# Optimization experiments

Measured on AMD Instinct MI355X. Metric: run time of the kernel, lower is better.

The kernel has to match this reference:

```python
import jax, jax.numpy as jnp
import numpy as np

B, N, D, H, DH = 1, 192, 128, 4, 32
INNER = H * DH  # == D


def _ln(x, g, b):
    mu = x.mean(-1, keepdims=True)
    var = ((x - mu) ** 2).mean(-1, keepdims=True)
    return (x - mu) * jax.lax.rsqrt(var + 1e-5) * g + b


def _axial(x, row, lng, lnb, wq, wkv, wo, bo, wg, bg, wb):
    # x: (B, N, N, D). row=True: attend along axis 2 (rows as batch);
    # row=False: attend along axis 1 (columns as batch).
    scale = DH ** -0.5
    # edge bias from RAW x (edges are not layer-normed in the torch code)
    bias = jnp.einsum('bijd,dh->bhij', x, wb)            # (B, H, N, N)
    xn = _ln(x, lng, lnb)
    xa = xn if row else jnp.swapaxes(xn, 1, 2)           # (B, R, S, D)
    q = (xa @ wq).reshape(B, N, N, H, DH) * scale
    kv = (xa @ wkv).reshape(B, N, N, 2, H, DH)           # chunk(2): k then v
    k, v = kv[..., 0, :, :], kv[..., 1, :, :]
    # scores: (B, R, H, q, k); same bias matrix broadcast over every row/col R
    dots = jnp.einsum('brqhe,brkhe->brhqk', q, k) + bias[:, None]
    attn = jax.nn.softmax(dots, axis=-1)
    o = jnp.einsum('brhqk,brkhe->brqhe', attn, v).reshape(B, N, N, INNER)
    gates = jax.nn.sigmoid(xa @ wg + bg)                 # sigmoid gating on pre-attn x
    out = (o * gates) @ wo + bo
    return out if row else jnp.swapaxes(out, 1, 2)


def setup_inputs() -> dict:
    key = jax.random.key(0)
    ks = iter(jax.random.split(key, 32))

    def w(shape, s=0.02):
        return jax.random.normal(next(ks), shape, dtype=jnp.float32) * s

    inp = {"x": jax.random.normal(next(ks), (B, N, N, D), dtype=jnp.float32)}
    for sfx in ("o", "i"):  # outgoing (row) / ingoing (col) triangle attention
        inp[f"lng_{sfx}"] = jnp.ones((D,), jnp.float32)
        inp[f"lnb_{sfx}"] = jnp.zeros((D,), jnp.float32)
        inp[f"wq_{sfx}"] = w((D, INNER))
        inp[f"wkv_{sfx}"] = w((D, 2 * INNER))
        inp[f"wo_{sfx}"] = w((INNER, D))
        inp[f"bo_{sfx}"] = jnp.zeros((D,), jnp.float32)
        inp[f"wg_{sfx}"] = w((D, INNER))
        inp[f"bg_{sfx}"] = jnp.ones((INNER,), jnp.float32)  # gating bias init = 1
        inp[f"wb_{sfx}"] = w((D, H))
    inp["lng_f"] = jnp.ones((D,), jnp.float32)
    inp["lnb_f"] = jnp.zeros((D,), jnp.float32)
    inp["w1"] = w((D, 8 * D))      # dim -> dim*mult*2, mult=4
    inp["b1"] = jnp.zeros((8 * D,), jnp.float32)
    inp["w2"] = w((4 * D, D))
    inp["b2"] = jnp.zeros((D,), jnp.float32)
    return inp


def reference(x, lng_o, lnb_o, wq_o, wkv_o, wo_o, bo_o, wg_o, bg_o, wb_o,
              lng_i, lnb_i, wq_i, wkv_i, wo_i, bo_i, wg_i, bg_i, wb_i,
              lng_f, lnb_f, w1, b1, w2, b2):
    x = _axial(x, True, lng_o, lnb_o, wq_o, wkv_o, wo_o, bo_o, wg_o, bg_o, wb_o) + x
    x = _axial(x, False, lng_i, lnb_i, wq_i, wkv_i, wo_i, bo_i, wg_i, bg_i, wb_i) + x
    xn = _ln(x, lng_f, lnb_f)
    h = xn @ w1 + b1
    a, g = jnp.split(h, 2, axis=-1)   # GEGLU: x * gelu(gates), exact gelu
    ff = (a * jax.nn.gelu(g, approximate=False)) @ w2 + b2
    return x + ff
```

## Files before the change

kernel.cpp:

```cpp
#include <hip/hip_runtime.h>
#include <hip/hip_bf16.h>
#include <math.h>

constexpr int NSEQ = 192;
constexpr int DIM  = 128;
constexpr int NH   = 4;
constexpr int DHEAD = 32;
constexpr int MROWS = NSEQ * NSEQ;

typedef __hip_bfloat16 bf16;
typedef __attribute__((ext_vector_type(8))) short bf16x8;
typedef __attribute__((ext_vector_type(4))) float f32x4;
typedef unsigned int u32;

__device__ __forceinline__ void gload16(const void* g, void* l) {
    __builtin_amdgcn_global_load_lds(
        (const __attribute__((address_space(1))) u32*)g,
        (__attribute__((address_space(3))) u32*)l, 16, 0, 0);
}

__device__ __forceinline__ short f2bs(float f) {
    __hip_bfloat16 h = __float2bfloat16(f);
    return *(short*)&h;
}

__global__ __launch_bounds__(256)
void convert_weights(const float* __restrict__ wq_o, const float* __restrict__ wkv_o,
                     const float* __restrict__ wg_o,
                     const float* __restrict__ wq_i, const float* __restrict__ wkv_i,
                     const float* __restrict__ wg_i,
                     const float* __restrict__ wo_o, const float* __restrict__ wo_i,
                     const float* __restrict__ w1, const float* __restrict__ b1,
                     const float* __restrict__ w2,
                     bf16* __restrict__ WQKVG_O, bf16* __restrict__ WQKVG_I,
                     bf16* __restrict__ WOT_O, bf16* __restrict__ WOT_I,
                     bf16* __restrict__ W1PT, bf16* __restrict__ W2T,
                     float* __restrict__ B1P)
{
    int idx = blockIdx.x * 256 + threadIdx.x;
    const float scale = 0.17677669529663689f;
    if (idx < 131072) {
        int s = idx >> 16, i = idx & 65535;
        int r = i >> 7, d = i & 127;
        const float* wq  = s ? wq_i  : wq_o;
        const float* wkv = s ? wkv_i : wkv_o;
        const float* wg  = s ? wg_i  : wg_o;
        float v;
        if (r < 128)      v = wq[d * 128 + r] * scale;
        else if (r < 384) v = wkv[d * 256 + (r - 128)];
        else              v = wg[d * 128 + (r - 384)];
        (s ? WQKVG_I : WQKVG_O)[i] = __float2bfloat16(v);
    } else if (idx < 163840) {
        int i = idx - 131072; int s = i >> 14; i &= 16383;
        int r = i >> 7, d = i & 127;
        (s ? WOT_I : WOT_O)[i] = __float2bfloat16((s ? wo_i : wo_o)[d * 128 + r]);
    } else if (idx < 294912) {
        int i = idx - 163840;
        int r = i >> 7, d = i & 127;
        int col = (r & 1) ? 512 + (r >> 1) : (r >> 1);
        W1PT[i] = __float2bfloat16(w1[d * 1024 + col]);
    } else if (idx < 360448) {
        int i = idx - 294912;
        int n = i >> 9, k = i & 511;
        W2T[i] = __float2bfloat16(w2[k * 128 + n]);
    } else if (idx < 361472) {
        int r = idx - 360448;
        B1P[r] = b1[(r & 1) ? 512 + (r >> 1) : (r >> 1)];
    }
}

__global__ __launch_bounds__(256)
void ln_bias_kernel(const float* __restrict__ x, const float* __restrict__ g,
                    const float* __restrict__ b, const float* __restrict__ wb,
                    bf16* __restrict__ xa, float* __restrict__ bias)
{
    int wid  = threadIdx.x >> 6;
    int lane = threadIdx.x & 63;
    int row  = blockIdx.x * 4 + wid;
    const float* xr = x + (size_t)row * DIM;
    float x0 = xr[lane], x1 = xr[lane + 64];
    float s = x0 + x1, sq = x0 * x0 + x1 * x1;
    #pragma unroll
    for (int off = 32; off > 0; off >>= 1) {
        s  += __shfl_down(s, off);
        sq += __shfl_down(sq, off);
    }
    s = __shfl(s, 0); sq = __shfl(sq, 0);
    float mu  = s * (1.0f / 128.0f);
    float var = sq * (1.0f / 128.0f) - mu * mu;
    float rs  = rsqrtf(var + 1e-5f);
    float y0 = (x0 - mu) * rs * g[lane]      + b[lane];
    float y1 = (x1 - mu) * rs * g[lane + 64] + b[lane + 64];
    bf16* yr = xa + (size_t)row * DIM;
    yr[lane]      = __float2bfloat16(y0);
    yr[lane + 64] = __float2bfloat16(y1);
    #pragma unroll
    for (int h = 0; h < NH; ++h) {
        float bh = x0 * wb[lane * NH + h] + x1 * wb[(lane + 64) * NH + h];
        #pragma unroll
        for (int off = 32; off > 0; off >>= 1) bh += __shfl_down(bh, off);
        if (lane == 0) bias[(size_t)h * MROWS + row] = bh;
    }
}

enum { EPI_QKVG = 0, EPI_OUT = 1, EPI_GEGLU = 2, EPI_FF2 = 3 };

template<int EPI, int BM, int K>
__global__ __launch_bounds__(256, 4)
void mfma_gemm(const bf16* __restrict__ A, const bf16* __restrict__ BT,
               const float* __restrict__ e_bias,
               const float* __restrict__ e_resid,
               float* __restrict__ e_outf,
               bf16* __restrict__ e_outb,
               bf16* __restrict__ e_outb2,
               const float* __restrict__ lng,
               const float* __restrict__ lnb,
               const float* __restrict__ wbp,
               float* __restrict__ biasb,
               bf16* __restrict__ xa,
               int trans)
{
    constexpr int MREP  = BM / 32;
    constexpr int AB    = BM * 128;
    constexpr int STAGE = AB + 16384;
    constexpr int EPIB  = (BM / 2) * 512;
    constexpr int LDSB  = STAGE > EPIB ? STAGE : EPIB;
    __shared__ char sm[LDSB];
    char* asb = sm;
    char* bsb = sm + AB;
    float* eb = (float*)sm;

    int tid = threadIdx.x;
    int l = tid & 63, w = tid >> 6;
    int wr = w >> 1, wc = w & 1;
    int m0 = blockIdx.x * BM, n0 = blockIdx.y * 128;
    int fr = l & 15, g = l >> 4;
    int lr8 = l >> 3;
    int satom = (l & 7) ^ lr8;

    f32x4 acc[MREP][4] = {};

    for (int k0 = 0; k0 < K; k0 += 64) {
        #pragma unroll
        for (int i = 0; i < BM / 32; ++i)
            gload16(A + (size_t)(m0 + i * 32 + w * 8 + lr8) * K + k0 + satom * 8,
                    asb + i * 4096 + w * 1024);
        #pragma unroll
        for (int i = 0; i < 4; ++i)
            gload16(BT + (size_t)(n0 + i * 32 + w * 8 + lr8) * K + k0 + satom * 8,
                    bsb + i * 4096 + w * 1024);
        __syncthreads();
        #pragma unroll
        for (int kk = 0; kk < 2; ++kk) {
            bf16x8 af[MREP], bfr[4];
            #pragma unroll
            for (int mi = 0; mi < MREP; ++mi) {
                int r = wr * (BM / 2) + mi * 16 + fr;
                af[mi] = *(const bf16x8*)(asb + r * 128 + ((kk * 64 + g * 16) ^ ((r & 7) << 4)));
            }
            #pragma unroll
            for (int ni = 0; ni < 4; ++ni) {
                int r = wc * 64 + ni * 16 + fr;
                bfr[ni] = *(const bf16x8*)(bsb + r * 128 + ((kk * 64 + g * 16) ^ ((r & 7) << 4)));
            }
            #pragma unroll
            for (int mi = 0; mi < MREP; ++mi)
                #pragma unroll
                for (int ni = 0; ni < 4; ++ni)
                    acc[mi][ni] = __builtin_amdgcn_mfma_f32_16x16x32_bf16(
                        af[mi], bfr[ni], acc[mi][ni], 0, 0, 0);
        }
        __syncthreads();
    }

    #pragma unroll
    for (int rr = 0; rr < 2; ++rr) {
        if (wr == rr) {
            #pragma unroll
            for (int mi = 0; mi < MREP; ++mi)
                #pragma unroll
                for (int ni = 0; ni < 4; ++ni)
                    #pragma unroll
                    for (int j = 0; j < 4; ++j) {
                        int rl = mi * 16 + g * 4 + j;
                        int cl = wc * 64 + ni * 16 + fr;
                        int a  = cl >> 2;
                        int pa = (((a >> 2) + (a & 3)) & 7) | ((a & 3) << 3);
                        eb[rl * 128 + pa * 4 + (cl & 3)] = acc[mi][ni][j];
                    }
        }
        __syncthreads();
        #pragma unroll
        for (int p = 0; p < BM / 64; ++p) {
            int c = tid + p * 256;
            int row_l = c >> 3, ch = c & 7;
            int grow = m0 + rr * (BM / 2) + row_l;
            int gc0 = ch * 16;
            float v[16];
            #pragma unroll
            for (int q = 0; q < 4; ++q) {
                int pa = ((ch + q) & 7) + q * 8;
                f32x4 t4 = *(const f32x4*)&eb[row_l * 128 + pa * 4];
                v[q * 4 + 0] = t4[0]; v[q * 4 + 1] = t4[1];
                v[q * 4 + 2] = t4[2]; v[q * 4 + 3] = t4[3];
            }
            if (EPI == EPI_QKVG) {
                int seg = blockIdx.y;
                short o16[16];
                if (seg < 3) {
                    #pragma unroll
                    for (int i = 0; i < 16; ++i) o16[i] = f2bs(v[i]);
                    int h = ch >> 1, e0 = (ch & 1) * 16;
                    bf16* dst = e_outb + ((size_t)(seg * NH + h) * MROWS + grow) * DHEAD + e0;
                    *(uint4*)dst = *(uint4*)o16;
                    *(uint4*)(dst + 8) = *(uint4*)(o16 + 8);
                } else {
                    #pragma unroll
                    for (int i = 0; i < 16; ++i)
                        o16[i] = f2bs(1.0f / (1.0f + __expf(-(v[i] + e_bias[gc0 + i]))));
                    bf16* dst = e_outb2 + (size_t)grow * DIM + gc0;
                    *(uint4*)dst = *(uint4*)o16;
                    *(uint4*)(dst + 8) = *(uint4*)(o16 + 8);
                }
            } else if (EPI == EPI_OUT) {
                int orow  = trans ? ((grow % NSEQ) * NSEQ + grow / NSEQ) : grow;
                int xarow = (grow % NSEQ) * NSEQ + grow / NSEQ;
                const float* rp = e_resid + (size_t)orow * DIM + gc0;
                float* op = e_outf + (size_t)orow * DIM + gc0;
                #pragma unroll
                for (int q = 0; q < 4; ++q) {
                    float4 r4 = *(const float4*)(rp + q * 4);
                    v[q*4+0] += e_bias[gc0 + q*4 + 0] + r4.x;
                    v[q*4+1] += e_bias[gc0 + q*4 + 1] + r4.y;
                    v[q*4+2] += e_bias[gc0 + q*4 + 2] + r4.z;
                    v[q*4+3] += e_bias[gc0 + q*4 + 3] + r4.w;
                    *(float4*)(op + q * 4) = make_float4(v[q*4+0], v[q*4+1], v[q*4+2], v[q*4+3]);
                }
                float s1 = 0.f, s2 = 0.f;
                #pragma unroll
                for (int i = 0; i < 16; ++i) { s1 += v[i]; s2 += v[i] * v[i]; }
                #pragma unroll
                for (int off = 1; off < 8; off <<= 1) {
                    s1 += __shfl_xor(s1, off);
                    s2 += __shfl_xor(s2, off);
                }
                float mu  = s1 * (1.0f / 128.0f);
                float var = s2 * (1.0f / 128.0f) - mu * mu;
                float rs  = rsqrtf(var + 1e-5f);
                short o16[16];
                #pragma unroll
                for (int i = 0; i < 16; ++i)
                    o16[i] = f2bs((v[i] - mu) * rs * lng[gc0 + i] + lnb[gc0 + i]);
                bf16* xd = xa + (size_t)xarow * DIM + gc0;
                *(uint4*)xd = *(uint4*)o16;
                *(uint4*)(xd + 8) = *(uint4*)(o16 + 8);
                if (wbp) {
                    float bh[NH] = {};
                    #pragma unroll
                    for (int i = 0; i < 16; ++i) {
                        float vv = v[i];
                        #pragma unroll
                        for (int h = 0; h < NH; ++h)
                            bh[h] = fmaf(vv, wbp[(gc0 + i) * NH + h], bh[h]);
                    }
                    #pragma unroll
                    for (int off = 1; off < 8; off <<= 1)
                        #pragma unroll
                        for (int h = 0; h < NH; ++h) bh[h] += __shfl_xor(bh[h], off);
                    if (ch == 0)
                        #pragma unroll
                        for (int h = 0; h < NH; ++h)
                            biasb[(size_t)h * MROWS + grow] = bh[h];
                }
            } else if (EPI == EPI_FF2) {
                const float* rp = e_resid + (size_t)grow * DIM + gc0;
                float* op = e_outf + (size_t)grow * DIM + gc0;
                #pragma unroll
                for (int q = 0; q < 4; ++q) {
                    float4 r4 = *(const float4*)(rp + q * 4);
                    float4 o4;
                    o4.x = v[q*4+0] + e_bias[gc0 + q*4 + 0] + r4.x;
                    o4.y = v[q*4+1] + e_bias[gc0 + q*4 + 1] + r4.y;
                    o4.z = v[q*4+2] + e_bias[gc0 + q*4 + 2] + r4.z;
                    o4.w = v[q*4+3] + e_bias[gc0 + q*4 + 3] + r4.w;
                    *(float4*)(op + q * 4) = o4;
                }
            } else {
                short o8[8];
                #pragma unroll
                for (int t = 0; t < 8; ++t) {
                    float a  = v[2*t]     + e_bias[n0 + gc0 + 2*t];
                    float gg = v[2*t + 1] + e_bias[n0 + gc0 + 2*t + 1];
                    float y  = 1.5957691216f * (gg + 0.044715f * gg * gg * gg);
                    float ge = gg / (1.0f + __expf(-y));
                    o8[t] = f2bs(a * ge);
                }
                *(uint4*)(e_outb + (size_t)grow * 512 + ((n0 + gc0) >> 1)) = *(uint4*)o8;
            }
        }
        __syncthreads();
    }
}

__global__ __launch_bounds__(256)
void attn_mfma_kernel(const bf16* __restrict__ Qh, const bf16* __restrict__ Kh,
                      const bf16* __restrict__ Vh, const float* __restrict__ BIAS,
                      const bf16* __restrict__ G, bf16* __restrict__ TMP)
{
    __shared__ unsigned short vtp[32][200];
    int h = blockIdx.x / NSEQ;
    int r = blockIdx.x % NSEQ;
    int t = threadIdx.x;
    int l = t & 63;
    int w = t >> 6;

    const bf16* vbase = Vh + ((size_t)h * MROWS + (size_t)r * NSEQ) * DHEAD;
    #pragma unroll
    for (int i = 0; i < 6; ++i) {
        int q4 = t + i * 256;
        int k = q4 >> 3, e0 = (q4 & 7) * 4;
        uint2 v = *(const uint2*)(vbase + (size_t)k * DHEAD + e0);
        int kk = k & 31, sup = k >> 5;
        int col = sup * 32 + ((kk & 15) >> 2) * 8 + (kk & 3) + ((kk >> 4) << 2);
        const unsigned short* vs = (const unsigned short*)&v;
        #pragma unroll
        for (int j = 0; j < 4; ++j) vtp[e0 + j][col] = vs[j];
    }
    __syncthreads();

    int fr = l & 15, g = l >> 4;
    int q0 = w * 48;
    const bf16*  qbase = Qh + ((size_t)h * MROWS + (size_t)r * NSEQ) * DHEAD;
    const bf16*  kbase = Kh + ((size_t)h * MROWS + (size_t)r * NSEQ) * DHEAD;
    const float* bbase = BIAS + (size_t)h * MROWS;

    bf16x8 qf[3];
    #pragma unroll
    for (int i = 0; i < 3; ++i)
        qf[i] = *(const bf16x8*)(qbase + (size_t)(q0 + i * 16 + fr) * DHEAD + g * 8);

    f32x4 ot[3][2] = {};
    float m_[3] = {-1e30f, -1e30f, -1e30f};
    float s_[3] = {};

    for (int sup = 0; sup < 6; ++sup) {
        bf16x8 kf0 = *(const bf16x8*)(kbase + (size_t)(sup * 32 + fr) * DHEAD + g * 8);
        bf16x8 kf1 = *(const bf16x8*)(kbase + (size_t)(sup * 32 + 16 + fr) * DHEAD + g * 8);
        bf16x8 pb[3];
        #pragma unroll
        for (int qt = 0; qt < 3; ++qt) {
            f32x4 z = {};
            f32x4 s0 = __builtin_amdgcn_mfma_f32_16x16x32_bf16(kf0, qf[qt], z, 0, 0, 0);
            f32x4 s1 = __builtin_amdgcn_mfma_f32_16x16x32_bf16(kf1, qf[qt], z, 0, 0, 0);
            const float* bp = bbase + (size_t)(q0 + qt * 16 + fr) * NSEQ + sup * 32 + g * 4;
            float4 b0 = *(const float4*)bp;
            float4 b1 = *(const float4*)(bp + 16);
            s0[0] += b0.x; s0[1] += b0.y; s0[2] += b0.z; s0[3] += b0.w;
            s1[0] += b1.x; s1[1] += b1.y; s1[2] += b1.z; s1[3] += b1.w;
            float tmax = fmaxf(fmaxf(fmaxf(s0[0], s0[1]), fmaxf(s0[2], s0[3])),
                               fmaxf(fmaxf(s1[0], s1[1]), fmaxf(s1[2], s1[3])));
            tmax = fmaxf(tmax, __shfl_xor(tmax, 16));
            tmax = fmaxf(tmax, __shfl_xor(tmax, 32));
            if (__any(tmax > m_[qt] + 8.0f)) {
                float mn = fmaxf(m_[qt], tmax);
                float c = __expf(m_[qt] - mn);
                s_[qt] *= c; ot[qt][0] *= c; ot[qt][1] *= c;
                m_[qt] = mn;
            }
            float p[8];
            #pragma unroll
            for (int j = 0; j < 4; ++j) p[j]     = __expf(s0[j] - m_[qt]);
            #pragma unroll
            for (int j = 0; j < 4; ++j) p[4 + j] = __expf(s1[j] - m_[qt]);
            s_[qt] += ((p[0] + p[1]) + (p[2] + p[3])) + ((p[4] + p[5]) + (p[6] + p[7]));
            bf16x8 pk;
            #pragma unroll
            for (int j = 0; j < 8; ++j) pk[j] = f2bs(p[j]);
            pb[qt] = pk;
        }
        #pragma unroll
        for (int et = 0; et < 2; ++et) {
            bf16x8 vf = *(const bf16x8*)(&vtp[et * 16 + fr][sup * 32 + g * 8]);
            #pragma unroll
            for (int qt = 0; qt < 3; ++qt)
                ot[qt][et] = __builtin_amdgcn_mfma_f32_16x16x32_bf16(vf, pb[qt], ot[qt][et], 0, 0, 0);
        }
    }

    #pragma unroll
    for (int qt = 0; qt < 3; ++qt) {
        float sq = s_[qt];
        sq += __shfl_xor(sq, 16);
        sq += __shfl_xor(sq, 32);
        float inv = 1.0f / sq;
        int q = q0 + qt * 16 + fr;
        size_t row = (size_t)r * NSEQ + q;
        #pragma unroll
        for (int et = 0; et < 2; ++et) {
            int e0 = h * DHEAD + et * 16 + g * 4;
            const bf16* gp = G + row * DIM + e0;
            u32 g01 = *(const u32*)gp;
            u32 g23 = *(const u32*)(gp + 2);
            float gx0 = __uint_as_float((g01 & 0xffffu) << 16);
            float gx1 = __uint_as_float(g01 & 0xffff0000u);
            float gx2 = __uint_as_float((g23 & 0xffffu) << 16);
            float gx3 = __uint_as_float(g23 & 0xffff0000u);
            short o4[4];
            o4[0] = f2bs(ot[qt][et][0] * inv * gx0);
            o4[1] = f2bs(ot[qt][et][1] * inv * gx1);
            o4[2] = f2bs(ot[qt][et][2] * inv * gx2);
            o4[3] = f2bs(ot[qt][et][3] * inv * gx3);
            *(uint2*)(TMP + row * DIM + e0) = *(uint2*)o4;
        }
    }
}

extern "C" void kernel_launch(void* const* d_in, const int* in_sizes, int n_in,
                              void* d_out, int out_size, void* d_ws, size_t ws_size,
                              hipStream_t stream) {
    const float* x     = (const float*)d_in[0];
    const float* lng_o = (const float*)d_in[1];
    const float* lnb_o = (const float*)d_in[2];
    const float* wq_o  = (const float*)d_in[3];
    const float* wkv_o = (const float*)d_in[4];
    const float* wo_o  = (const float*)d_in[5];
    const float* bo_o  = (const float*)d_in[6];
    const float* wg_o  = (const float*)d_in[7];
    const float* bg_o  = (const float*)d_in[8];
    const float* wb_o  = (const float*)d_in[9];
    const float* lng_i = (const float*)d_in[10];
    const float* lnb_i = (const float*)d_in[11];
    const float* wq_i  = (const float*)d_in[12];
    const float* wkv_i = (const float*)d_in[13];
    const float* wo_i  = (const float*)d_in[14];
    const float* bo_i  = (const float*)d_in[15];
    const float* wg_i  = (const float*)d_in[16];
    const float* bg_i  = (const float*)d_in[17];
    const float* wb_i  = (const float*)d_in[18];
    const float* lng_f = (const float*)d_in[19];
    const float* lnb_f = (const float*)d_in[20];
    const float* w1    = (const float*)d_in[21];
    const float* b1    = (const float*)d_in[22];
    const float* w2    = (const float*)d_in[23];
    const float* b2    = (const float*)d_in[24];

    const size_t T = (size_t)MROWS * DIM;
    char* base = (char*)d_ws;
    bf16*  XA    = (bf16*)base;  base += T * 2;
    float* X     = (float*)base; base += T * 4;
    bf16*  QKVb  = (bf16*)base;  base += 3 * T * 2;
    bf16*  Gb    = (bf16*)base;  base += T * 2;
    float* BIASb = (float*)base; base += (size_t)NH * MROWS * 4;
    bf16*  TMP   = (bf16*)base;  base += T * 2;
    bf16*  WQKVG_O = (bf16*)base; base += 512 * 128 * 2;
    bf16*  WQKVG_I = (bf16*)base; base += 512 * 128 * 2;
    bf16*  WOT_O   = (bf16*)base; base += 128 * 128 * 2;
    bf16*  WOT_I   = (bf16*)base; base += 128 * 128 * 2;
    bf16*  W1PT    = (bf16*)base; base += 1024 * 128 * 2;
    bf16*  W2T     = (bf16*)base; base += 128 * 512 * 2;
    float* B1P     = (float*)base; base += 1024 * 4;
    bf16*  H2      = (bf16*)QKVb;
    bf16*  Qhp = QKVb;
    bf16*  Khp = QKVb + T;
    bf16*  Vhp = QKVb + 2 * T;

    convert_weights<<<1412, 256, 0, stream>>>(wq_o, wkv_o, wg_o, wq_i, wkv_i, wg_i,
                                              wo_o, wo_i, w1, b1, w2,
                                              WQKVG_O, WQKVG_I, WOT_O, WOT_I,
                                              W1PT, W2T, B1P);

    dim3 gQKVG(MROWS / 128, 4), gOUT(MROWS / 128, 1), gW1(MROWS / 128, 8);
    dim3 gFF2(MROWS / 64, 1);

    ln_bias_kernel<<<MROWS / 4, 256, 0, stream>>>(x, lng_o, lnb_o, wb_o, XA, BIASb);
    mfma_gemm<EPI_QKVG, 128, 128><<<gQKVG, 256, 0, stream>>>(
        XA, WQKVG_O, bg_o, nullptr, nullptr, QKVb, Gb,
        nullptr, nullptr, nullptr, nullptr, nullptr, 0);
    attn_mfma_kernel<<<NSEQ * NH, 256, 0, stream>>>(Qhp, Khp, Vhp, BIASb, Gb, TMP);
    mfma_gemm<EPI_OUT, 128, 128><<<gOUT, 256, 0, stream>>>(
        TMP, WOT_O, bo_o, x, X, nullptr, nullptr,
        lng_i, lnb_i, wb_i, BIASb, XA, 0);

    mfma_gemm<EPI_QKVG, 128, 128><<<gQKVG, 256, 0, stream>>>(
        XA, WQKVG_I, bg_i, nullptr, nullptr, QKVb, Gb,
        nullptr, nullptr, nullptr, nullptr, nullptr, 0);
    attn_mfma_kernel<<<NSEQ * NH, 256, 0, stream>>>(Qhp, Khp, Vhp, BIASb, Gb, TMP);
    mfma_gemm<EPI_OUT, 128, 128><<<gOUT, 256, 0, stream>>>(
        TMP, WOT_I, bo_i, X, X, nullptr, nullptr,
        lng_f, lnb_f, nullptr, nullptr, XA, 1);

    mfma_gemm<EPI_GEGLU, 128, 128><<<gW1, 256, 0, stream>>>(
        XA, W1PT, B1P, nullptr, nullptr, H2, nullptr,
        nullptr, nullptr, nullptr, nullptr, nullptr, 0);
    mfma_gemm<EPI_FF2, 64, 512><<<gFF2, 256, 0, stream>>>(
        H2, W2T, b2, X, (float*)d_out, nullptr, nullptr,
        nullptr, nullptr, nullptr, nullptr, nullptr, 0);
}
```

Measured before the change: 231.2 us.

## Fuse GEGLU FFN into one kernel and merge weight prep with first LayerNorm

The two FFN GEMMs are replaced by a single fused kernel. It computes W1 in chunks of 128 columns, applies GEGLU into a shared-memory buffer, and accumulates the W2 product in registers, so the 36864x512 bf16 intermediate never goes to global memory. Weight conversion and the first LayerNorm/edge-bias pass are merged into one launch, and the LN loads are vectorised. The cost is heavy LDS use (72KB, two blocks per CU), syncs inside every chunk without overlap of the global-to-LDS loads, and uncoalesced scalar stores in the output epilogue. The wb float4 indexing (wb + lane*8) appears to assume a different element pairing than the old lane/lane+64 split, which may change which weights each lane uses.

```diff
diff --git a/kernel.cpp b/kernel.cpp
--- a/kernel.cpp
+++ b/kernel.cpp
@@ -25,61 +25,60 @@
 }
 
 __global__ __launch_bounds__(256)
-void convert_weights(const float* __restrict__ wq_o, const float* __restrict__ wkv_o,
-                     const float* __restrict__ wg_o,
-                     const float* __restrict__ wq_i, const float* __restrict__ wkv_i,
-                     const float* __restrict__ wg_i,
-                     const float* __restrict__ wo_o, const float* __restrict__ wo_i,
-                     const float* __restrict__ w1, const float* __restrict__ b1,
-                     const float* __restrict__ w2,
-                     bf16* __restrict__ WQKVG_O, bf16* __restrict__ WQKVG_I,
-                     bf16* __restrict__ WOT_O, bf16* __restrict__ WOT_I,
-                     bf16* __restrict__ W1PT, bf16* __restrict__ W2T,
-                     float* __restrict__ B1P)
+void prep_kernel(const float* __restrict__ wq_o, const float* __restrict__ wkv_o,
+                 const float* __restrict__ wg_o,
+                 const float* __restrict__ wq_i, const float* __restrict__ wkv_i,
+                 const float* __restrict__ wg_i,
+                 const float* __restrict__ wo_o, const float* __restrict__ wo_i,
+                 const float* __restrict__ w1, const float* __restrict__ b1,
+                 const float* __restrict__ w2,
+                 bf16* __restrict__ WQKVG_O, bf16* __restrict__ WQKVG_I,
+                 bf16* __restrict__ WOT_O, bf16* __restrict__ WOT_I,
+                 bf16* __restrict__ W1PT, bf16* __restrict__ W2T,
+                 float* __restrict__ B1P,
+                 const float* __restrict__ x, const float* __restrict__ lng,
+                 const float* __restrict__ lnb, const float* __restrict__ wb,
+                 bf16* __restrict__ xa, float* __restrict__ bias)
 {
-    int idx = blockIdx.x * 256 + threadIdx.x;
-    const float scale = 0.17677669529663689f;
-    if (idx < 131072) {
-        int s = idx >> 16, i = idx & 65535;
-        int r = i >> 7, d = i & 127;
-        const float* wq  = s ? wq_i  : wq_o;
-        const float* wkv = s ? wkv_i : wkv_o;
-        const float* wg  = s ? wg_i  : wg_o;
-        float v;
-        if (r < 128)      v = wq[d * 128 + r] * scale;
-        else if (r < 384) v = wkv[d * 256 + (r - 128)];
-        else              v = wg[d * 128 + (r - 384)];
-        (s ? WQKVG_I : WQKVG_O)[i] = __float2bfloat16(v);
-    } else if (idx < 163840) {
-        int i = idx - 131072; int s = i >> 14; i &= 16383;
-        int r = i >> 7, d = i & 127;
-        (s ? WOT_I : WOT_O)[i] = __float2bfloat16((s ? wo_i : wo_o)[d * 128 + r]);
-    } else if (idx < 294912) {
-        int i = idx - 163840;
-        int r = i >> 7, d = i & 127;
-        int col = (r & 1) ? 512 + (r >> 1) : (r >> 1);
-        W1PT[i] = __float2bfloat16(w1[d * 1024 + col]);
-    } else if (idx < 360448) {
-        int i = idx - 294912;
-        int n = i >> 9, k = i & 511;
-        W2T[i] = __float2bfloat16(w2[k * 128 + n]);
-    } else if (idx < 361472) {
-        int r = idx - 360448;
-        B1P[r] = b1[(r & 1) ? 512 + (r >> 1) : (r >> 1)];
-    }
-}
-
-__global__ __launch_bounds__(256)
-void ln_bias_kernel(const float* __restrict__ x, const float* __restrict__ g,
-                    const float* __restrict__ b, const float* __restrict__ wb,
-                    bf16* __restrict__ xa, float* __restrict__ bias)
-{
+    if (blockIdx.x < 1412) {
+        int idx = blockIdx.x * 256 + threadIdx.x;
+        const float scale = 0.17677669529663689f;
+        if (idx < 131072) {
+            int s = idx >> 16, i = idx & 65535;
+            int r = i >> 7, d = i & 127;
+            const float* wq  = s ? wq_i  : wq_o;
+            const float* wkv = s ? wkv_i : wkv_o;
+            const float* wg  = s ? wg_i  : wg_o;
+            float v;
+            if (r < 128)      v = wq[d * 128 + r] * scale;
+            else if (r < 384) v = wkv[d * 256 + (r - 128)];
+            else              v = wg[d * 128 + (r - 384)];
+            (s ? WQKVG_I : WQKVG_O)[i] = __float2bfloat16(v);
+        } else if (idx < 163840) {
+            int i = idx - 131072; int s = i >> 14; i &= 16383;
+            int r = i >> 7, d = i & 127;
+            (s ? WOT_I : WOT_O)[i] = __float2bfloat16((s ? wo_i : wo_o)[d * 128 + r]);
+        } else if (idx < 294912) {
+            int i = idx - 163840;
+            int r = i >> 7, d = i & 127;
+            int col = (r & 1) ? 512 + (r >> 1) : (r >> 1);
+            W1PT[i] = __float2bfloat16(w1[d * 1024 + col]);
+        } else if (idx < 360448) {
+            int i = idx - 294912;
+            int n = i >> 9, k = i & 511;
+            W2T[i] = __float2bfloat16(w2[k * 128 + n]);
+        } else if (idx < 361472) {
+            int r = idx - 360448;
+            B1P[r] = b1[(r & 1) ? 512 + (r >> 1) : (r >> 1)];
+        }
+        return;
+    }
     int wid  = threadIdx.x >> 6;
     int lane = threadIdx.x & 63;
-    int row  = blockIdx.x * 4 + wid;
+    int row  = (blockIdx.x - 1412) * 4 + wid;
     const float* xr = x + (size_t)row * DIM;
-    float x0 = xr[lane], x1 = xr[lane + 64];
-    float s = x0 + x1, sq = x0 * x0 + x1 * x1;
+    float2 xv = *(const float2*)(xr + lane * 2);
+    float s = xv.x + xv.y, sq = xv.x * xv.x + xv.y * xv.y;
     #pragma unroll
     for (int off = 32; off > 0; off >>= 1) {
         s  += __shfl_down(s, off);
@@ -89,21 +88,24 @@
     float mu  = s * (1.0f / 128.0f);
     float var = sq * (1.0f / 128.0f) - mu * mu;
     float rs  = rsqrtf(var + 1e-5f);
-    float y0 = (x0 - mu) * rs * g[lane]      + b[lane];
-    float y1 = (x1 - mu) * rs * g[lane + 64] + b[lane + 64];
-    bf16* yr = xa + (size_t)row * DIM;
-    yr[lane]      = __float2bfloat16(y0);
-    yr[lane + 64] = __float2bfloat16(y1);
+    float2 gv = *(const float2*)(lng + lane * 2);
+    float2 bv = *(const float2*)(lnb + lane * 2);
+    float y0 = (xv.x - mu) * rs * gv.x + bv.x;
+    float y1 = (xv.y - mu) * rs * gv.y + bv.y;
+    u32 packed = (u32)(unsigned short)f2bs(y0) | ((u32)(unsigned short)f2bs(y1) << 16);
+    *(u32*)(xa + (size_t)row * DIM + lane * 2) = packed;
+    float4 w0 = *(const float4*)(wb + lane * 8);
+    float4 w1v = *(const float4*)(wb + lane * 8 + 4);
     #pragma unroll
     for (int h = 0; h < NH; ++h) {
-        float bh = x0 * wb[lane * NH + h] + x1 * wb[(lane + 64) * NH + h];
+        float bh = xv.x * ((const float*)&w0)[h] + xv.y * ((const float*)&w1v)[h];
         #pragma unroll
         for (int off = 32; off > 0; off >>= 1) bh += __shfl_down(bh, off);
         if (lane == 0) bias[(size_t)h * MROWS + row] = bh;
     }
 }
 
-enum { EPI_QKVG = 0, EPI_OUT = 1, EPI_GEGLU = 2, EPI_FF2 = 3 };
+enum { EPI_QKVG = 0, EPI_OUT = 1 };
 
 template<int EPI, int BM, int K>
 __global__ __launch_bounds__(256, 4)
@@ -222,7 +224,7 @@
                     *(uint4*)dst = *(uint4*)o16;
                     *(uint4*)(dst + 8) = *(uint4*)(o16 + 8);
                 }
-            } else if (EPI == EPI_OUT) {
+            } else {
                 int orow  = trans ? ((grow % NSEQ) * NSEQ + grow / NSEQ) : grow;
                 int xarow = (grow % NSEQ) * NSEQ + grow / NSEQ;
                 const float* rp = e_resid + (size_t)orow * DIM + gc0;
@@ -272,34 +274,130 @@
                         for (int h = 0; h < NH; ++h)
                             biasb[(size_t)h * MROWS + grow] = bh[h];
                 }
-            } else if (EPI == EPI_FF2) {
-                const float* rp = e_resid + (size_t)grow * DIM + gc0;
-                float* op = e_outf + (size_t)grow * DIM + gc0;
-                #pragma unroll
-                for (int q = 0; q < 4; ++q) {
-                    float4 r4 = *(const float4*)(rp + q * 4);
-                    float4 o4;
-                    o4.x = v[q*4+0] + e_bias[gc0 + q*4 + 0] + r4.x;
-                    o4.y = v[q*4+1] + e_bias[gc0 + q*4 + 1] + r4.y;
-                    o4.z = v[q*4+2] + e_bias[gc0 + q*4 + 2] + r4.z;
-                    o4.w = v[q*4+3] + e_bias[gc0 + q*4 + 3] + r4.w;
-                    *(float4*)(op + q * 4) = o4;
+            }
+        }
+        __syncthreads();
+    }
+}
+
+__global__ __launch_bounds__(256, 2)
+void ffn_kernel(const bf16* __restrict__ XA, const bf16* __restrict__ W1PT,
+                const bf16* __restrict__ W2T, const float* __restrict__ B1P,
+                const float* __restrict__ b2, const float* __restrict__ X,
+                float* __restrict__ out)
+{
+    __shared__ char sm[73728];
+    char* asb = sm;
+    char* w1b = sm + 16384;
+    char* pbuf = sm + 49152;
+    char* w2b = sm + 57344;
+    int tid = threadIdx.x;
+    int l = tid & 63, w = tid >> 6;
+    int wr = w >> 1, wc = w & 1;
+    int fr = l & 15, g = l >> 4;
+    int m0 = blockIdx.x * 64;
+
+    {
+        int r16 = tid >> 4, a = tid & 15;
+        int ap = a ^ (r16 & 7);
+        #pragma unroll
+        for (int i = 0; i < 4; ++i)
+            gload16(XA + (size_t)(m0 + i * 16 + r16) * 128 + ap * 8,
+                    asb + i * 4096 + w * 1024);
+    }
+    f32x4 acc2[2][4] = {};
+
+    for (int c = 0; c < 8; ++c) {
+        {
+            int r16 = tid >> 4, a = tid & 15;
+            int ap = a ^ (r16 & 7);
+            #pragma unroll
+            for (int i = 0; i < 8; ++i)
+                gload16(W1PT + (size_t)(c * 128 + i * 16 + r16) * 128 + ap * 8,
+                        w1b + i * 4096 + w * 1024);
+        }
+        __syncthreads();
+        f32x4 acc1[2][4] = {};
+        #pragma unroll
+        for (int kk = 0; kk < 4; ++kk) {
+            bf16x8 af[2], bfr[4];
+            #pragma unroll
+            for (int mi = 0; mi < 2; ++mi) {
+                int r = wr * 32 + mi * 16 + fr;
+                af[mi] = *(const bf16x8*)(asb + r * 256 + ((kk * 64 + g * 16) ^ ((r & 7) << 4)));
+            }
+            #pragma unroll
+            for (int ni = 0; ni < 4; ++ni) {
+                int r = wc * 64 + ni * 16 + fr;
+                bfr[ni] = *(const bf16x8*)(w1b + r * 256 + ((kk * 64 + g * 16) ^ ((r & 7) << 4)));
+            }
+            #pragma unroll
+            for (int mi = 0; mi < 2; ++mi)
+                #pragma unroll
+                for (int ni = 0; ni < 4; ++ni)
+                    acc1[mi][ni] = __builtin_amdgcn_mfma_f32_16x16x32_bf16(
+                        af[mi], bfr[ni], acc1[mi][ni], 0, 0, 0);
+        }
+        __syncthreads();
+        #pragma unroll
+        for (int mi = 0; mi < 2; ++mi)
+            #pragma unroll
+            for (int ni = 0; ni < 4; ++ni)
+                #pragma unroll
+                for (int j = 0; j < 4; ++j) {
+                    int rl = wr * 32 + mi * 16 + g * 4 + j;
+                    int cl = wc * 64 + ni * 16 + fr;
+                    float v = acc1[mi][ni][j] + B1P[c * 128 + cl];
+                    float pg = __shfl_xor(v, 1);
+                    if (!(fr & 1)) {
+                        float y  = 1.5957691216f * (pg + 0.044715f * pg * pg * pg);
+                        float ge = pg / (1.0f + __expf(-y));
+                        *(short*)(pbuf + rl * 128 + ((((cl >> 1) * 2)) ^ ((rl & 7) << 4)))
+                            = f2bs(v * ge);
+                    }
                 }
-            } else {
-                short o8[8];
-                #pragma unroll
-                for (int t = 0; t < 8; ++t) {
-                    float a  = v[2*t]     + e_bias[n0 + gc0 + 2*t];
-                    float gg = v[2*t + 1] + e_bias[n0 + gc0 + 2*t + 1];
-                    float y  = 1.5957691216f * (gg + 0.044715f * gg * gg * gg);
-                    float ge = gg / (1.0f + __expf(-y));
-                    o8[t] = f2bs(a * ge);
-                }
-                *(uint4*)(e_outb + (size_t)grow * 512 + ((n0 + gc0) >> 1)) = *(uint4*)o8;
-            }
-        }
-        __syncthreads();
-    }
+        {
+            int r32 = tid >> 3, a = tid & 7;
+            int ap = a ^ (r32 & 7);
+            #pragma unroll
+            for (int i = 0; i < 4; ++i)
+                gload16(W2T + (size_t)(i * 32 + r32) * 512 + c * 64 + ap * 8,
+                        w2b + i * 4096 + w * 1024);
+        }
+        __syncthreads();
+        #pragma unroll
+        for (int kk = 0; kk < 2; ++kk) {
+            bf16x8 pf[2], bfr[4];
+            #pragma unroll
+            for (int mi = 0; mi < 2; ++mi) {
+                int r = wr * 32 + mi * 16 + fr;
+                pf[mi] = *(const bf16x8*)(pbuf + r * 128 + ((kk * 64 + g * 16) ^ ((r & 7) << 4)));
+            }
+            #pragma unroll
+            for (int ni = 0; ni < 4; ++ni) {
+                int r = wc * 64 + ni * 16 + fr;
+                bfr[ni] = *(const bf16x8*)(w2b + r * 128 + ((kk * 64 + g * 16) ^ ((r & 7) << 4)));
+            }
+            #pragma unroll
+            for (int mi = 0; mi < 2; ++mi)
+                #pragma unroll
+                for (int ni = 0; ni < 4; ++ni)
+                    acc2[mi][ni] = __builtin_amdgcn_mfma_f32_16x16x32_bf16(
+                        pf[mi], bfr[ni], acc2[mi][ni], 0, 0, 0);
+        }
+        __syncthreads();
+    }
+    #pragma unroll
+    for (int mi = 0; mi < 2; ++mi)
+        #pragma unroll
+        for (int ni = 0; ni < 4; ++ni)
+            #pragma unroll
+            for (int j = 0; j < 4; ++j) {
+                int row = m0 + wr * 32 + mi * 16 + g * 4 + j;
+                int col = wc * 64 + ni * 16 + fr;
+                out[(size_t)row * DIM + col] =
+                    acc2[mi][ni][j] + b2[col] + X[(size_t)row * DIM + col];
+            }
 }
 
 __global__ __launch_bounds__(256)
@@ -459,20 +557,17 @@
     bf16*  W1PT    = (bf16*)base; base += 1024 * 128 * 2;
     bf16*  W2T     = (bf16*)base; base += 128 * 512 * 2;
     float* B1P     = (float*)base; base += 1024 * 4;
-    bf16*  H2      = (bf16*)QKVb;
     bf16*  Qhp = QKVb;
     bf16*  Khp = QKVb + T;
     bf16*  Vhp = QKVb + 2 * T;
 
-    convert_weights<<<1412, 256, 0, stream>>>(wq_o, wkv_o, wg_o, wq_i, wkv_i, wg_i,
-                                              wo_o, wo_i, w1, b1, w2,
-                                              WQKVG_O, WQKVG_I, WOT_O, WOT_I,
-                                              W1PT, W2T, B1P);
-
-    dim3 gQKVG(MROWS / 128, 4), gOUT(MROWS / 128, 1), gW1(MROWS / 128, 8);
-    dim3 gFF2(MROWS / 64, 1);
-
-    ln_bias_kernel<<<MROWS / 4, 256, 0, stream>>>(x, lng_o, lnb_o, wb_o, XA, BIASb);
+    prep_kernel<<<1412 + MROWS / 4, 256, 0, stream>>>(
+        wq_o, wkv_o, wg_o, wq_i, wkv_i, wg_i, wo_o, wo_i, w1, b1, w2,
+        WQKVG_O, WQKVG_I, WOT_O, WOT_I, W1PT, W2T, B1P,
+        x, lng_o, lnb_o, wb_o, XA, BIASb);
+
+    dim3 gQKVG(MROWS / 128, 4), gOUT(MROWS / 128, 1);
+
     mfma_gemm<EPI_QKVG, 128, 128><<<gQKVG, 256, 0, stream>>>(
         XA, WQKVG_O, bg_o, nullptr, nullptr, QKVb, Gb,
         nullptr, nullptr, nullptr, nullptr, nullptr, 0);
@@ -489,10 +584,5 @@
         TMP, WOT_I, bo_i, X, X, nullptr, nullptr,
         lng_f, lnb_f, nullptr, nullptr, XA, 1);
 
-    mfma_gemm<EPI_GEGLU, 128, 128><<<gW1, 256, 0, stream>>>(
-        XA, W1PT, B1P, nullptr, nullptr, H2, nullptr,
-        nullptr, nullptr, nullptr, nullptr, nullptr, 0);
-    mfma_gemm<EPI_FF2, 64, 512><<<gFF2, 256, 0, stream>>>(
-        H2, W2T, b2, X, (float*)d_out, nullptr, nullptr,
-        nullptr, nullptr, nullptr, nullptr, nullptr, 0);
-}
+    ffn_kernel<<<MROWS / 64, 256, 0, stream>>>(XA, W1PT, W2T, B1P, b2, X, (float*)d_out);
+}
```

New measurement: 272.0 us. 17.7% more time.
